# Kernel optimization log

Hardware: AMD Instinct MI355X
Metric: run time of the kernel (lower is better)

## Reference

```python
import jax, jax.numpy as jnp
import numpy as np

WINDOW = (8, 8)
NUM_HEADS = 12


def setup_inputs() -> dict:
    key = jax.random.key(0)
    k0, k1, k2 = jax.random.split(key, 3)
    B_, H, W, C = 8, 64, 64, 768
    x = jax.random.normal(k0, (B_, H * W, C), dtype=jnp.float32)
    qkv_w = jax.random.normal(k1, (3 * C, C), dtype=jnp.float32) * 0.02
    qkv_b = jnp.zeros((3 * C,), dtype=jnp.float32)
    proj_w = jax.random.normal(k2, (C, C), dtype=jnp.float32) * 0.02
    proj_b = jnp.zeros((C,), dtype=jnp.float32)
    return {"x": x, "qkv_w": qkv_w, "qkv_b": qkv_b,
            "proj_w": proj_w, "proj_b": proj_b, "H": H, "W": W}


def reference(x, qkv_w, qkv_b, proj_w, proj_b, H, W):
    ws0, ws1 = WINDOW
    nh = NUM_HEADS
    B_, N, C = x.shape
    hd = C // nh
    scale = hd ** (-0.5)

    x = x.reshape(B_, H, W, C)
    # pad bottom/right so H, W divisible by window size (static Python ints)
    pad_b = (ws0 - H % ws0) % ws0
    pad_r = (ws1 - W % ws1) % ws1
    x = jnp.pad(x, ((0, 0), (0, pad_b), (0, pad_r), (0, 0)))
    Hp, Wp = H + pad_b, W + pad_r

    # window partition: (B, Hp, Wp, C) -> (B*nW, ws0*ws1, C)
    xw = (x.reshape(B_, Hp // ws0, ws0, Wp // ws1, ws1, C)
            .transpose(0, 1, 3, 2, 4, 5)
            .reshape(-1, ws0 * ws1, C))
    Bw, Nw = xw.shape[0], xw.shape[1]

    # fused qkv projection
    qkv = xw @ qkv_w.T + qkv_b                       # (Bw, Nw, 3C)
    qkv = qkv.reshape(Bw, Nw, 3, nh, hd).transpose(2, 0, 3, 1, 4)
    q, k, v = qkv[0], qkv[1], qkv[2]                 # (Bw, nh, Nw, hd)

    attn = jax.nn.softmax((q * scale) @ jnp.swapaxes(k, -2, -1), axis=-1)
    out = (attn @ v).transpose(0, 2, 1, 3).reshape(Bw, Nw, C)
    out = out @ proj_w.T + proj_b

    # window reverse: (B*nW, ws0*ws1, C) -> (B, Hp, Wp, C)
    out = (out.reshape(B_, Hp // ws0, Wp // ws1, ws0, ws1, C)
              .transpose(0, 1, 3, 2, 4, 5)
              .reshape(B_, Hp, Wp, C))
    out = out[:, :H, :W, :]
    return out.reshape(B_, H * W, C)
```

## Files before the change

kernel.cpp:

```cpp
#include <hip/hip_runtime.h>
#include <stdint.h>

typedef __attribute__((ext_vector_type(8))) __bf16 bf16x8;
typedef __attribute__((ext_vector_type(4))) float f32x4;
typedef __attribute__((ext_vector_type(8))) unsigned short u16x8;
typedef __attribute__((ext_vector_type(2))) unsigned int u32x2;

__device__ __forceinline__ unsigned f2bf(float f) {
  union { float f; unsigned u; } v; v.f = f;
  return (v.u + 0x7FFFu + ((v.u >> 16) & 1u)) >> 16;
}

__device__ __forceinline__ void gload16(const void* g, void* l) {
  __builtin_amdgcn_global_load_lds(
      (const __attribute__((address_space(1))) void*)g,
      (__attribute__((address_space(3))) void*)l, 16, 0, 0);
}

__global__ __launch_bounds__(256) void pack_x_kernel(const float* __restrict__ x,
                                                     unsigned short* __restrict__ xw) {
  int idx = blockIdx.x * 256 + threadIdx.x;
  int m = idx / 96;
  int p = idx - m * 96;
  int win = m >> 6, tok = m & 63;
  int b = win >> 6, wh = (win >> 3) & 7, ww = win & 7;
  int r = tok >> 3, c = tok & 7;
  size_t xoff = ((size_t)b * 4096 + (wh * 8 + r) * 64 + (ww * 8 + c)) * 768 + p * 8;
  const float* src = x + xoff;
  u16x8 o;
#pragma unroll
  for (int j = 0; j < 8; ++j) o[j] = (unsigned short)f2bf(src[j]);
  *(u16x8*)(xw + (size_t)m * 768 + p * 8) = o;
}

__global__ __launch_bounds__(256) void pack_w_kernel(const float* __restrict__ qkvw,
                                                     const float* __restrict__ projw,
                                                     unsigned short* __restrict__ wq,
                                                     unsigned short* __restrict__ wp) {
  int idx = blockIdx.x * 256 + threadIdx.x;
  const float* src;
  unsigned short* dst;
  if (idx < 221184) { src = qkvw + (size_t)idx * 8; dst = wq + (size_t)idx * 8; }
  else { int i2 = idx - 221184; src = projw + (size_t)i2 * 8; dst = wp + (size_t)i2 * 8; }
  u16x8 o;
#pragma unroll
  for (int j = 0; j < 8; ++j) o[j] = (unsigned short)f2bf(src[j]);
  *(u16x8*)dst = o;
}

template <int N>
__global__ __launch_bounds__(512, 2) void gemm256_kernel(
    const unsigned short* __restrict__ A, const unsigned short* __restrict__ Bm,
    const float* __restrict__ bias, unsigned short* __restrict__ C) {
  constexpr int K = 768;
  constexpr int NT = K / 32;
  constexpr int NBN = N / 256;
  extern __shared__ char smem[];

  const int tid = threadIdx.x;
  const int wave = tid >> 6;
  const int lane = tid & 63;
  const int wm = wave >> 2;
  const int wn = wave & 3;

  const int cpx = gridDim.x >> 3;
  const int bid = (blockIdx.x & 7) * cpx + (blockIdx.x >> 3);
  const int tm = (bid / NBN) * 256;
  const int tn = (bid % NBN) * 256;

  const int c0 = tid, c1 = 512 + tid;
  const int r0 = c0 >> 2, r1 = c1 >> 2;
  const int g0 = ((c0 & 3) ^ ((c0 >> 3) & 3)) * 8;
  const int g1 = ((c1 & 3) ^ ((c1 >> 3) & 3)) * 8;
  const unsigned short* gA0 = A + (size_t)(tm + r0) * K + g0;
  const unsigned short* gA1 = A + (size_t)(tm + r1) * K + g1;
  const unsigned short* gB0 = Bm + (size_t)(tn + r0) * K + g0;
  const unsigned short* gB1 = Bm + (size_t)(tn + r1) * K + g1;
  const int ldsA0 = wave * 1024;
  const int ldsA1 = 8192 + wave * 1024;
  const int ldsB0 = 16384 + wave * 1024;
  const int ldsB1 = 24576 + wave * 1024;

  const int lrow = lane & 15;
  const int lg8 = ((lane >> 4) ^ ((lane >> 1) & 3)) * 8;

  {
    char* s0 = smem;
    char* s1 = smem + 32768;
    gload16(gA0, s0 + ldsA0); gload16(gA1, s0 + ldsA1);
    gload16(gB0, s0 + ldsB0); gload16(gB1, s0 + ldsB1);
    gload16(gA0 + 32, s1 + ldsA0); gload16(gA1 + 32, s1 + ldsA1);
    gload16(gB0 + 32, s1 + ldsB0); gload16(gB1 + 32, s1 + ldsB1);
  }
  asm volatile("s_waitcnt vmcnt(4)" ::: "memory");
  asm volatile("s_barrier" ::: "memory");

  f32x4 acc[8][4] = {};

  bf16x8 a0[4], b[4];
  {
    const unsigned short* s0 = (const unsigned short*)smem;
#pragma unroll
    for (int mi = 0; mi < 4; ++mi)
      a0[mi] = *(const bf16x8*)(s0 + (wm * 128 + mi * 16 + lrow) * 32 + lg8);
#pragma unroll
    for (int ni = 0; ni < 4; ++ni)
      b[ni] = *(const bf16x8*)(s0 + 8192 + (wn * 64 + ni * 16 + lrow) * 32 + lg8);
  }

#pragma unroll
  for (int t = 0; t < NT; ++t) {
    const unsigned short* sAt = (const unsigned short*)(smem + ((t & 3) << 15));

    if (t + 2 < NT) {
      char* sb = smem + (((t + 2) & 3) << 15);
      gload16(gA0 + (t + 2) * 32, sb + ldsA0);
      gload16(gA1 + (t + 2) * 32, sb + ldsA1);
    }
    bf16x8 a1[4];
#pragma unroll
    for (int mi = 0; mi < 4; ++mi)
      a1[mi] = *(const bf16x8*)(sAt + (wm * 128 + 64 + mi * 16 + lrow) * 32 + lg8);

    __builtin_amdgcn_s_setprio(1);
#pragma unroll
    for (int mi = 0; mi < 4; ++mi)
#pragma unroll
      for (int ni = 0; ni < 4; ++ni)
        acc[mi][ni] = __builtin_amdgcn_mfma_f32_16x16x32_bf16(b[ni], a0[mi], acc[mi][ni], 0, 0, 0);
    __builtin_amdgcn_s_setprio(0);

    if (t + 2 < NT) {
      char* sb = smem + (((t + 2) & 3) << 15);
      gload16(gB0 + (t + 2) * 32, sb + ldsB0);
      gload16(gB1 + (t + 2) * 32, sb + ldsB1);
    }
    if (t < NT - 2)
      asm volatile("s_waitcnt vmcnt(4)" ::: "memory");
    else if (t == NT - 2)
      asm volatile("s_waitcnt vmcnt(0)" ::: "memory");
    if (t < NT - 1)
      asm volatile("s_barrier" ::: "memory");

    bf16x8 a0n[4], bn[4];
    if (t + 1 < NT) {
      const unsigned short* sN = (const unsigned short*)(smem + (((t + 1) & 3) << 15));
#pragma unroll
      for (int mi = 0; mi < 4; ++mi)
        a0n[mi] = *(const bf16x8*)(sN + (wm * 128 + mi * 16 + lrow) * 32 + lg8);
#pragma unroll
      for (int ni = 0; ni < 4; ++ni)
        bn[ni] = *(const bf16x8*)(sN + 8192 + (wn * 64 + ni * 16 + lrow) * 32 + lg8);
    }

    __builtin_amdgcn_s_setprio(1);
#pragma unroll
    for (int mi = 0; mi < 4; ++mi)
#pragma unroll
      for (int ni = 0; ni < 4; ++ni)
        acc[4 + mi][ni] = __builtin_amdgcn_mfma_f32_16x16x32_bf16(b[ni], a1[mi], acc[4 + mi][ni], 0, 0, 0);
    __builtin_amdgcn_s_setprio(0);

#pragma unroll
    for (int i = 0; i < 4; ++i) { a0[i] = a0n[i]; b[i] = bn[i]; }
  }

  const int erow = tm + wm * 128 + (lane & 15);
  const int ecol = tn + wn * 64 + ((lane >> 4) << 2);
  f32x4 bv[4];
#pragma unroll
  for (int ni = 0; ni < 4; ++ni) bv[ni] = *(const f32x4*)&bias[ecol + ni * 16];
#pragma unroll
  for (int mi = 0; mi < 8; ++mi) {
    unsigned short* rowp = C + (size_t)(erow + mi * 16) * N;
#pragma unroll
    for (int ni = 0; ni < 4; ++ni) {
      f32x4 v = acc[mi][ni];
      u32x2 pk;
      pk.x = f2bf(v[0] + bv[ni][0]) | (f2bf(v[1] + bv[ni][1]) << 16);
      pk.y = f2bf(v[2] + bv[ni][2]) | (f2bf(v[3] + bv[ni][3]) << 16);
      *(u32x2*)(rowp + ecol + ni * 16) = pk;
    }
  }
}

__global__ __launch_bounds__(256, 3) void gemm128_proj_kernel(
    const unsigned short* __restrict__ A, const unsigned short* __restrict__ Bm,
    const float* __restrict__ bias, float* __restrict__ out) {
  constexpr int K = 768;
  constexpr int NT = K / 32;
  constexpr int N = 768;
  constexpr int NBN = N / 128;
  __shared__ char smem[49152];

  const int tid = threadIdx.x;
  const int wave = tid >> 6;
  const int lane = tid & 63;
  const int wmr = wave >> 1;
  const int wnc = wave & 1;

  const int cpx = gridDim.x >> 3;
  const int bid = (blockIdx.x & 7) * cpx + (blockIdx.x >> 3);
  const int tm = (bid / NBN) * 128;
  const int tn = (bid % NBN) * 128;

  const int srow0 = wave * 16 + (lane >> 2);
  const int sgl = ((lane & 3) ^ ((lane >> 3) & 3)) * 8;
  const unsigned short* gA0 = A + (size_t)(tm + srow0) * K + sgl;
  const unsigned short* gA1 = A + (size_t)(tm + 64 + srow0) * K + sgl;
  const unsigned short* gB0 = Bm + (size_t)(tn + srow0) * K + sgl;
  const unsigned short* gB1 = Bm + (size_t)(tn + 64 + srow0) * K + sgl;
  const int ldsW = wave * 1024;

#define STAGE(s, slot) do {                                        \
    char* d_ = smem + (slot) * 16384;                              \
    gload16(gA0 + (s) * 32, d_ + ldsW);                            \
    gload16(gA1 + (s) * 32, d_ + 4096 + ldsW);                     \
    gload16(gB0 + (s) * 32, d_ + 8192 + ldsW);                     \
    gload16(gB1 + (s) * 32, d_ + 12288 + ldsW);                    \
  } while (0)

  const int lrow = lane & 15;
  const int pgb = (((lane >> 4) ^ ((lane >> 1) & 3)) << 4);

  STAGE(0, 0);
  STAGE(1, 1);
  asm volatile("s_waitcnt vmcnt(4)" ::: "memory");
  asm volatile("s_barrier" ::: "memory");

  f32x4 acc[4][4] = {};

  bf16x8 a0[2], b[4];
  {
    const char* aB = smem + (wmr * 64 + lrow) * 64 + pgb;
    const char* bB = smem + 8192 + (wnc * 64 + lrow) * 64 + pgb;
#pragma unroll
    for (int mi = 0; mi < 2; ++mi) a0[mi] = *(const bf16x8*)(aB + mi * 1024);
#pragma unroll
    for (int ni = 0; ni < 4; ++ni) b[ni] = *(const bf16x8*)(bB + ni * 1024);
  }

#pragma unroll
  for (int t = 0; t < NT; ++t) {
    const char* cb = smem + (t % 3) * 16384;
    const char* aB = cb + (wmr * 64 + lrow) * 64 + pgb;

    if (t + 2 < NT) STAGE(t + 2, (t + 2) % 3);
    bf16x8 a1[2];
#pragma unroll
    for (int mi = 0; mi < 2; ++mi)
      a1[mi] = *(const bf16x8*)(aB + (2 + mi) * 1024);

    __builtin_amdgcn_s_setprio(1);
#pragma unroll
    for (int mi = 0; mi < 2; ++mi)
#pragma unroll
      for (int ni = 0; ni < 4; ++ni)
        acc[mi][ni] = __builtin_amdgcn_mfma_f32_16x16x32_bf16(b[ni], a0[mi], acc[mi][ni], 0, 0, 0);
    __builtin_amdgcn_s_setprio(0);

    if (t + 2 < NT)
      asm volatile("s_waitcnt vmcnt(4)" ::: "memory");
    else if (t == NT - 2)
      asm volatile("s_waitcnt vmcnt(0)" ::: "memory");
    if (t + 1 < NT)
      asm volatile("s_barrier" ::: "memory");

    bf16x8 a0n[2], bn[4];
    if (t + 1 < NT) {
      const char* nb = smem + ((t + 1) % 3) * 16384;
      const char* aN = nb + (wmr * 64 + lrow) * 64 + pgb;
      const char* bN = nb + 8192 + (wnc * 64 + lrow) * 64 + pgb;
#pragma unroll
      for (int mi = 0; mi < 2; ++mi) a0n[mi] = *(const bf16x8*)(aN + mi * 1024);
#pragma unroll
      for (int ni = 0; ni < 4; ++ni) bn[ni] = *(const bf16x8*)(bN + ni * 1024);
    }

    __builtin_amdgcn_s_setprio(1);
#pragma unroll
    for (int mi = 0; mi < 2; ++mi)
#pragma unroll
      for (int ni = 0; ni < 4; ++ni)
        acc[2 + mi][ni] = __builtin_amdgcn_mfma_f32_16x16x32_bf16(b[ni], a1[mi], acc[2 + mi][ni], 0, 0, 0);
    __builtin_amdgcn_s_setprio(0);

#pragma unroll
    for (int i = 0; i < 2; ++i) a0[i] = a0n[i];
#pragma unroll
    for (int i = 0; i < 4; ++i) b[i] = bn[i];
  }
#undef STAGE

  const int erow = tm + wmr * 64 + (lane & 15);
  const int ecol = tn + wnc * 64 + ((lane >> 4) << 2);
  f32x4 bv[4];
#pragma unroll
  for (int ni = 0; ni < 4; ++ni) bv[ni] = *(const f32x4*)&bias[ecol + ni * 16];
#pragma unroll
  for (int mi = 0; mi < 4; ++mi) {
    int m = erow + mi * 16;
    int win = m >> 6, tok = m & 63;
    int bb = win >> 6, wh = (win >> 3) & 7, ww = win & 7;
    int rr = tok >> 3, cc = tok & 7;
    float* op = out + ((size_t)bb * 4096 + (wh * 8 + rr) * 64 + (ww * 8 + cc)) * 768;
#pragma unroll
    for (int ni = 0; ni < 4; ++ni) {
      f32x4 o = acc[mi][ni] + bv[ni];
      *(f32x4*)(op + ecol + ni * 16) = o;
    }
  }
}

__global__ __launch_bounds__(64) void attn_kernel(const unsigned short* __restrict__ qkv,
                                                  unsigned short* __restrict__ attnout) {
  __shared__ unsigned short sQ[64 * 64];
  __shared__ unsigned short sK[64 * 64];
  __shared__ unsigned short sVT[64 * 64];
  const int lane = threadIdx.x;
  const int win = blockIdx.x / 12;
  const int head = blockIdx.x - win * 12;
  const size_t row0 = (size_t)win * 64;
  const int qoff = head * 64, koff = 768 + head * 64, voff = 1536 + head * 64;

#pragma unroll
  for (int i = 0; i < 8; ++i) {
    int e = lane + i * 64;
    int row = e >> 3, cb = (e & 7) * 8;
    gload16(qkv + (row0 + row) * 2304 + qoff + cb, (char*)sQ + i * 1024);
    gload16(qkv + (row0 + row) * 2304 + koff + cb, (char*)sK + i * 1024);
  }
  {
    const unsigned short* gv = qkv + (row0 + lane) * 2304 + voff;
#pragma unroll
    for (int j = 0; j < 8; ++j) {
      u16x8 v = *(const u16x8*)(gv + j * 8);
#pragma unroll
      for (int d = 0; d < 8; ++d) sVT[(j * 8 + d) * 64 + lane] = v[d];
    }
  }
  __syncthreads();

  const int lrow = lane & 15;
  const int lkb = (lane >> 4) * 8;

  f32x4 s[4][4] = {};
#pragma unroll
  for (int ks = 0; ks < 2; ++ks) {
    bf16x8 qf[4], kf[4];
#pragma unroll
    for (int mi = 0; mi < 4; ++mi) qf[mi] = *(const bf16x8*)&sQ[(mi * 16 + lrow) * 64 + ks * 32 + lkb];
#pragma unroll
    for (int ni = 0; ni < 4; ++ni) kf[ni] = *(const bf16x8*)&sK[(ni * 16 + lrow) * 64 + ks * 32 + lkb];
#pragma unroll
    for (int mi = 0; mi < 4; ++mi)
#pragma unroll
      for (int ni = 0; ni < 4; ++ni)
        s[mi][ni] = __builtin_amdgcn_mfma_f32_16x16x32_bf16(qf[mi], kf[ni], s[mi][ni], 0, 0, 0);
  }

  float p[4][4][4];
#pragma unroll
  for (int mi = 0; mi < 4; ++mi) {
#pragma unroll
    for (int r = 0; r < 4; ++r) {
      float v0 = s[mi][0][r] * 0.125f, v1 = s[mi][1][r] * 0.125f;
      float v2 = s[mi][2][r] * 0.125f, v3 = s[mi][3][r] * 0.125f;
      float mx = fmaxf(fmaxf(v0, v1), fmaxf(v2, v3));
      mx = fmaxf(mx, __shfl_xor(mx, 1));
      mx = fmaxf(mx, __shfl_xor(mx, 2));
      mx = fmaxf(mx, __shfl_xor(mx, 4));
      mx = fmaxf(mx, __shfl_xor(mx, 8));
      float e0 = __expf(v0 - mx), e1 = __expf(v1 - mx);
      float e2 = __expf(v2 - mx), e3 = __expf(v3 - mx);
      float sm = e0 + e1 + e2 + e3;
      sm += __shfl_xor(sm, 1);
      sm += __shfl_xor(sm, 2);
      sm += __shfl_xor(sm, 4);
      sm += __shfl_xor(sm, 8);
      float inv = 1.0f / sm;
      p[mi][0][r] = e0 * inv; p[mi][1][r] = e1 * inv;
      p[mi][2][r] = e2 * inv; p[mi][3][r] = e3 * inv;
    }
  }

  __syncthreads();
#pragma unroll
  for (int mi = 0; mi < 4; ++mi)
#pragma unroll
    for (int ni = 0; ni < 4; ++ni)
#pragma unroll
      for (int r = 0; r < 4; ++r)
        sK[(mi * 16 + (lane >> 4) * 4 + r) * 64 + ni * 16 + lrow] = (unsigned short)f2bf(p[mi][ni][r]);
  __syncthreads();

  f32x4 o[4][4] = {};
#pragma unroll
  for (int ks = 0; ks < 2; ++ks) {
    bf16x8 pf[4], vf[4];
#pragma unroll
    for (int mi = 0; mi < 4; ++mi) pf[mi] = *(const bf16x8*)&sK[(mi * 16 + lrow) * 64 + ks * 32 + lkb];
#pragma unroll
    for (int ni = 0; ni < 4; ++ni) vf[ni] = *(const bf16x8*)&sVT[(ni * 16 + lrow) * 64 + ks * 32 + lkb];
#pragma unroll
    for (int mi = 0; mi < 4; ++mi)
#pragma unroll
      for (int ni = 0; ni < 4; ++ni)
        o[mi][ni] = __builtin_amdgcn_mfma_f32_16x16x32_bf16(pf[mi], vf[ni], o[mi][ni], 0, 0, 0);
  }

#pragma unroll
  for (int mi = 0; mi < 4; ++mi)
#pragma unroll
    for (int ni = 0; ni < 4; ++ni) {
      int col = head * 64 + ni * 16 + lrow;
#pragma unroll
      for (int r = 0; r < 4; ++r) {
        int trow = mi * 16 + (lane >> 4) * 4 + r;
        attnout[(row0 + trow) * 768 + col] = (unsigned short)f2bf(o[mi][ni][r]);
      }
    }
}

extern "C" void kernel_launch(void* const* d_in, const int* in_sizes, int n_in,
                              void* d_out, int out_size, void* d_ws, size_t ws_size,
                              hipStream_t stream) {
  (void)in_sizes; (void)n_in; (void)out_size; (void)ws_size;
  const float* x = (const float*)d_in[0];
  const float* qkv_w = (const float*)d_in[1];
  const float* qkv_b = (const float*)d_in[2];
  const float* proj_w = (const float*)d_in[3];
  const float* proj_b = (const float*)d_in[4];
  float* out = (float*)d_out;

  char* ws = (char*)d_ws;
  unsigned short* xw   = (unsigned short*)(ws);
  unsigned short* qkvB = (unsigned short*)(ws + 50331648);
  unsigned short* wq   = (unsigned short*)(ws + 50331648 + 150994944);
  unsigned short* wp   = (unsigned short*)(ws + 50331648 + 150994944 + 3538944);

  (void)hipFuncSetAttribute((const void*)(gemm256_kernel<2304>),
                            hipFuncAttributeMaxDynamicSharedMemorySize, 131072);

  pack_x_kernel<<<12288, 256, 0, stream>>>(x, xw);
  pack_w_kernel<<<1152, 256, 0, stream>>>(qkv_w, proj_w, wq, wp);
  gemm256_kernel<2304><<<1152, 512, 131072, stream>>>(xw, wq, qkv_b, qkvB);
  attn_kernel<<<6144, 64, 0, stream>>>(qkvB, xw);
  gemm128_proj_kernel<<<1536, 256, 0, stream>>>(xw, wp, proj_b, out);
}
```

Baseline: 285.2 us.

## Use 1024-thread blocks in QKV GEMM with 64-row-per-wave tiles

The 256x256 QKV GEMM tile is now split across 16 waves instead of 8. Each wave computes a 64x64 sub-tile with half the accumulators, and each thread issues one A and one B LDS-direct load per stage. The cross-iteration register prefetch of fragments is dropped in favour of plain per-iteration LDS reads. This aims to raise the number of waves that hide latency, at the cost of more LDS traffic per MFMA and less software pipelining.

```diff
diff --git a/kernel.cpp b/kernel.cpp
--- a/kernel.cpp
+++ b/kernel.cpp
@@ -49,7 +49,7 @@
 }
 
 template <int N>
-__global__ __launch_bounds__(512, 2) void gemm256_kernel(
+__global__ __launch_bounds__(1024, 4) void gemm256_kernel(
     const unsigned short* __restrict__ A, const unsigned short* __restrict__ Bm,
     const float* __restrict__ bias, unsigned short* __restrict__ C) {
   constexpr int K = 768;
@@ -68,110 +68,77 @@
   const int tm = (bid / NBN) * 256;
   const int tn = (bid % NBN) * 256;
 
-  const int c0 = tid, c1 = 512 + tid;
-  const int r0 = c0 >> 2, r1 = c1 >> 2;
-  const int g0 = ((c0 & 3) ^ ((c0 >> 3) & 3)) * 8;
-  const int g1 = ((c1 & 3) ^ ((c1 >> 3) & 3)) * 8;
-  const unsigned short* gA0 = A + (size_t)(tm + r0) * K + g0;
-  const unsigned short* gA1 = A + (size_t)(tm + r1) * K + g1;
-  const unsigned short* gB0 = Bm + (size_t)(tn + r0) * K + g0;
-  const unsigned short* gB1 = Bm + (size_t)(tn + r1) * K + g1;
-  const int ldsA0 = wave * 1024;
-  const int ldsA1 = 8192 + wave * 1024;
-  const int ldsB0 = 16384 + wave * 1024;
-  const int ldsB1 = 24576 + wave * 1024;
+  const int srow = tid >> 2;
+  const int sgl = ((tid & 3) ^ ((tid >> 3) & 3)) * 8;
+  const unsigned short* gA = A + (size_t)(tm + srow) * K + sgl;
+  const unsigned short* gB = Bm + (size_t)(tn + srow) * K + sgl;
+  const int ldsW = wave * 1024;
+
+#define STAGE(s, slot) do {                                        \
+    char* d_ = smem + ((slot) << 15);                              \
+    gload16(gA + (s) * 32, d_ + ldsW);                             \
+    gload16(gB + (s) * 32, d_ + 16384 + ldsW);                     \
+  } while (0)
 
   const int lrow = lane & 15;
-  const int lg8 = ((lane >> 4) ^ ((lane >> 1) & 3)) * 8;
-
-  {
-    char* s0 = smem;
-    char* s1 = smem + 32768;
-    gload16(gA0, s0 + ldsA0); gload16(gA1, s0 + ldsA1);
-    gload16(gB0, s0 + ldsB0); gload16(gB1, s0 + ldsB1);
-    gload16(gA0 + 32, s1 + ldsA0); gload16(gA1 + 32, s1 + ldsA1);
-    gload16(gB0 + 32, s1 + ldsB0); gload16(gB1 + 32, s1 + ldsB1);
-  }
-  asm volatile("s_waitcnt vmcnt(4)" ::: "memory");
+  const int pgb = (((lane >> 4) ^ ((lane >> 1) & 3)) << 4);
+
+  STAGE(0, 0);
+  STAGE(1, 1);
+  asm volatile("s_waitcnt vmcnt(2)" ::: "memory");
   asm volatile("s_barrier" ::: "memory");
 
-  f32x4 acc[8][4] = {};
-
-  bf16x8 a0[4], b[4];
-  {
-    const unsigned short* s0 = (const unsigned short*)smem;
-#pragma unroll
-    for (int mi = 0; mi < 4; ++mi)
-      a0[mi] = *(const bf16x8*)(s0 + (wm * 128 + mi * 16 + lrow) * 32 + lg8);
-#pragma unroll
-    for (int ni = 0; ni < 4; ++ni)
-      b[ni] = *(const bf16x8*)(s0 + 8192 + (wn * 64 + ni * 16 + lrow) * 32 + lg8);
-  }
+  f32x4 acc[4][4] = {};
 
 #pragma unroll
   for (int t = 0; t < NT; ++t) {
-    const unsigned short* sAt = (const unsigned short*)(smem + ((t & 3) << 15));
-
-    if (t + 2 < NT) {
-      char* sb = smem + (((t + 2) & 3) << 15);
-      gload16(gA0 + (t + 2) * 32, sb + ldsA0);
-      gload16(gA1 + (t + 2) * 32, sb + ldsA1);
-    }
-    bf16x8 a1[4];
-#pragma unroll
-    for (int mi = 0; mi < 4; ++mi)
-      a1[mi] = *(const bf16x8*)(sAt + (wm * 128 + 64 + mi * 16 + lrow) * 32 + lg8);
+    const char* sb = smem + ((t & 3) << 15);
+    const char* aB = sb + (wm * 64 + lrow) * 64 + pgb;
+    const char* bB = sb + 16384 + (wn * 64 + lrow) * 64 + pgb;
+
+    if (t + 2 < NT) STAGE(t + 2, (t + 2) & 3);
+
+    bf16x8 b[4], a[2];
+#pragma unroll
+    for (int ni = 0; ni < 4; ++ni) b[ni] = *(const bf16x8*)(bB + ni * 1024);
+#pragma unroll
+    for (int mi = 0; mi < 2; ++mi) a[mi] = *(const bf16x8*)(aB + mi * 1024);
 
     __builtin_amdgcn_s_setprio(1);
 #pragma unroll
-    for (int mi = 0; mi < 4; ++mi)
-#pragma unroll
-      for (int ni = 0; ni < 4; ++ni)
-        acc[mi][ni] = __builtin_amdgcn_mfma_f32_16x16x32_bf16(b[ni], a0[mi], acc[mi][ni], 0, 0, 0);
+    for (int mi = 0; mi < 2; ++mi)
+#pragma unroll
+      for (int ni = 0; ni < 4; ++ni)
+        acc[mi][ni] = __builtin_amdgcn_mfma_f32_16x16x32_bf16(b[ni], a[mi], acc[mi][ni], 0, 0, 0);
     __builtin_amdgcn_s_setprio(0);
 
-    if (t + 2 < NT) {
-      char* sb = smem + (((t + 2) & 3) << 15);
-      gload16(gB0 + (t + 2) * 32, sb + ldsB0);
-      gload16(gB1 + (t + 2) * 32, sb + ldsB1);
-    }
+#pragma unroll
+    for (int mi = 0; mi < 2; ++mi) a[mi] = *(const bf16x8*)(aB + (2 + mi) * 1024);
+
+    __builtin_amdgcn_s_setprio(1);
+#pragma unroll
+    for (int mi = 0; mi < 2; ++mi)
+#pragma unroll
+      for (int ni = 0; ni < 4; ++ni)
+        acc[2 + mi][ni] = __builtin_amdgcn_mfma_f32_16x16x32_bf16(b[ni], a[mi], acc[2 + mi][ni], 0, 0, 0);
+    __builtin_amdgcn_s_setprio(0);
+
     if (t < NT - 2)
-      asm volatile("s_waitcnt vmcnt(4)" ::: "memory");
+      asm volatile("s_waitcnt vmcnt(2)" ::: "memory");
     else if (t == NT - 2)
       asm volatile("s_waitcnt vmcnt(0)" ::: "memory");
-    if (t < NT - 1)
+    if (t + 1 < NT)
       asm volatile("s_barrier" ::: "memory");
-
-    bf16x8 a0n[4], bn[4];
-    if (t + 1 < NT) {
-      const unsigned short* sN = (const unsigned short*)(smem + (((t + 1) & 3) << 15));
-#pragma unroll
-      for (int mi = 0; mi < 4; ++mi)
-        a0n[mi] = *(const bf16x8*)(sN + (wm * 128 + mi * 16 + lrow) * 32 + lg8);
-#pragma unroll
-      for (int ni = 0; ni < 4; ++ni)
-        bn[ni] = *(const bf16x8*)(sN + 8192 + (wn * 64 + ni * 16 + lrow) * 32 + lg8);
-    }
-
-    __builtin_amdgcn_s_setprio(1);
-#pragma unroll
-    for (int mi = 0; mi < 4; ++mi)
-#pragma unroll
-      for (int ni = 0; ni < 4; ++ni)
-        acc[4 + mi][ni] = __builtin_amdgcn_mfma_f32_16x16x32_bf16(b[ni], a1[mi], acc[4 + mi][ni], 0, 0, 0);
-    __builtin_amdgcn_s_setprio(0);
-
-#pragma unroll
-    for (int i = 0; i < 4; ++i) { a0[i] = a0n[i]; b[i] = bn[i]; }
-  }
-
-  const int erow = tm + wm * 128 + (lane & 15);
+  }
+#undef STAGE
+
+  const int erow = tm + wm * 64 + (lane & 15);
   const int ecol = tn + wn * 64 + ((lane >> 4) << 2);
   f32x4 bv[4];
 #pragma unroll
   for (int ni = 0; ni < 4; ++ni) bv[ni] = *(const f32x4*)&bias[ecol + ni * 16];
 #pragma unroll
-  for (int mi = 0; mi < 8; ++mi) {
+  for (int mi = 0; mi < 4; ++mi) {
     unsigned short* rowp = C + (size_t)(erow + mi * 16) * N;
 #pragma unroll
     for (int ni = 0; ni < 4; ++ni) {
@@ -444,7 +411,7 @@
 
   pack_x_kernel<<<12288, 256, 0, stream>>>(x, xw);
   pack_w_kernel<<<1152, 256, 0, stream>>>(qkv_w, proj_w, wq, wp);
-  gemm256_kernel<2304><<<1152, 512, 131072, stream>>>(xw, wq, qkv_b, qkvB);
+  gemm256_kernel<2304><<<1152, 1024, 131072, stream>>>(xw, wq, qkv_b, qkvB);
   attn_kernel<<<6144, 64, 0, stream>>>(qkvB, xw);
   gemm128_proj_kernel<<<1536, 256, 0, stream>>>(xw, wp, proj_b, out);
 }
```

Result: no change. 286.2 us (+0.3%).
